# Performance work log

Hardware: AMD Instinct MI355X
Metric: run time of the kernel (lower is better)

The kernel has to match this reference:

```python
import jax, jax.numpy as jnp
import numpy as np

B, S, NB, D, H = 4, 512, 32, 512, 8

def setup_inputs() -> dict:
    key = jax.random.key(0)
    ks = jax.random.split(key, 8)
    sc = 1.0 / np.sqrt(D)
    return {
        "query": jax.random.normal(ks[0], (B, S, NB, D), dtype=jnp.float32),
        "key": jax.random.normal(ks[1], (B, S, NB, D), dtype=jnp.float32),
        "value": jax.random.normal(ks[2], (B, S, NB, D), dtype=jnp.float32),
        "padding_mask": jnp.zeros((B, S, NB), dtype=jnp.float32),
        "wq": jax.random.normal(ks[3], (D, D), dtype=jnp.float32) * sc,
        "bq": jnp.zeros((D,), dtype=jnp.float32),
        "wk": jax.random.normal(ks[4], (D, D), dtype=jnp.float32) * sc,
        "bk": jnp.zeros((D,), dtype=jnp.float32),
        "wv": jax.random.normal(ks[5], (D, D), dtype=jnp.float32) * sc,
        "bv": jnp.zeros((D,), dtype=jnp.float32),
        "nhead": H,
    }

def reference(query, key, value, padding_mask, wq, bq, wk, bk, wv, bv, nhead):
    b, s, nb, d = query.shape
    dh = d // nhead
    # Linear projections (torch Linear: x @ W.T + b)
    Q = query @ wq.T + bq
    K = key @ wk.T + bk
    V = value @ wv.T + bv
    # [B, S, Nb, H, dh] -> [B, H, S, Nb, dh]
    def split_heads(x):
        return x.reshape(b, s, nb, nhead, dh).transpose(0, 3, 1, 2, 4)
    Qh, Kh, Vh = split_heads(Q), split_heads(K), split_heads(V)
    # attention over the block axis per (batch, head, seq position)
    logits = jnp.einsum('bhsnd,bhsmd->bhsnm', Qh, Kh) / jnp.sqrt(jnp.float32(dh))
    # additive mask [B, S, Nb] -> [B, 1, S, 1, Nb]
    logits = logits + padding_mask[:, None, :, None, :]
    attn_weight = jax.nn.softmax(logits, axis=-1)  # [B,H,S,Nb,Nb]
    attn_output = jnp.einsum('bhsnm,bhsmd->bhsnd', attn_weight, Vh)
    # [B,H,S,Nb,dh] -> [B,S,Nb,H,dh] -> [B,S,Nb,D]
    attn_output = attn_output.transpose(0, 2, 3, 1, 4).reshape(b, s, nb, d)
    return (attn_output, attn_weight)
```

## Files before the change

### kernel.cpp

```cpp
#include <hip/hip_runtime.h>
#include <hip/hip_bf16.h>


#define NBD (32 * 512)
#define XH_STRIDE 260
#define XH_BYTES (32 * XH_STRIDE * 2)

typedef __bf16 bf16x8 __attribute__((ext_vector_type(8)));
typedef float f32x16 __attribute__((ext_vector_type(16)));

__device__ __forceinline__ unsigned f2b(float f) {
  union { float f; unsigned u; } v;
  v.f = f;
  return (v.u + 0x7fffu + ((v.u >> 16) & 1u)) >> 16;
}

__device__ __forceinline__ f32x16 mfma32(uint4 a, uint4 b, f32x16 c) {
  union { uint4 u; bf16x8 v; } ua, ub;
  ua.u = a;
  ub.u = b;
  return __builtin_amdgcn_mfma_f32_32x32x16_bf16(ua.v, ub.v, c, 0, 0, 0);
}

__device__ __forceinline__ uint4 ld_lds_64x2(const unsigned short* p, unsigned byteoff) {
  const char* c = (const char*)p;
  uint2 lo = *(const uint2*)(c + byteoff);
  uint2 hi = *(const uint2*)(c + byteoff + 8);
  uint4 r;
  r.x = lo.x; r.y = lo.y; r.z = hi.x; r.w = hi.y;
  return r;
}

__device__ __forceinline__ uint4 frag_cd(const unsigned* CP, int qb, int half) {
  const unsigned s0 = __shfl_xor(CP[qb + 0], 32);
  const unsigned s1 = __shfl_xor(CP[qb + 1], 32);
  const unsigned s2 = __shfl_xor(CP[qb + 2], 32);
  const unsigned s3 = __shfl_xor(CP[qb + 3], 32);
  uint4 f;
  f.x = half ? s2 : CP[qb + 0];
  f.y = half ? s3 : CP[qb + 1];
  f.z = half ? CP[qb + 2] : s0;
  f.w = half ? CP[qb + 3] : s1;
  return f;
}

__global__ void wconv_kernel(const float* __restrict__ wq,
                             const float* __restrict__ wk,
                             const float* __restrict__ wv,
                             uint4* __restrict__ out) {
  const int g = blockIdx.x * blockDim.x + threadIdx.x;
  const int m = g >> 15;
  const int j = g & 32767;
  const int l31 = j & 31;
  const int half = (j >> 5) & 1;
  const int k = (j >> 6) & 31;
  const int tile = j >> 11;
  const float* src = (m == 0) ? wq : (m == 1) ? wk : wv;
  const float4* p = (const float4*)(src + (size_t)(tile * 32 + l31) * 512 + k * 16 + half * 8);
  float4 f0 = p[0], f1 = p[1];
  uint4 o;
  o.x = f2b(f0.x) | (f2b(f0.y) << 16);
  o.y = f2b(f0.z) | (f2b(f0.w) << 16);
  o.z = f2b(f1.x) | (f2b(f1.y) << 16);
  o.w = f2b(f1.z) | (f2b(f1.w) << 16);
  out[g] = o;
}

__global__ __launch_bounds__(512, 4)
void mhba_kernel(const float* __restrict__ q_in, const float* __restrict__ k_in,
                 const float* __restrict__ v_in, const float* __restrict__ mask,
                 const float* __restrict__ bq, const float* __restrict__ bk,
                 const float* __restrict__ bv,
                 const uint4* __restrict__ wpk,
                 float* __restrict__ out_attn,
                 float* __restrict__ out_w) {
  __shared__ unsigned short Xs[2][32 * XH_STRIDE];
  __shared__ __align__(16) char SCR[8][4352];

  const int bs = blockIdx.x;
  const int tid = threadIdx.x;
  const int lane = tid & 63;
  const int h = tid >> 6;
  const int l31 = lane & 31;
  const int half = lane >> 5;

  char* scr = &SCR[h][0];
  const float* srcs[3] = {k_in, q_in, v_in};

  unsigned QT[2][8], VP[2][8];
  const unsigned abase = (unsigned)(l31 * (XH_STRIDE * 2) + half * 16);

  float4 st[4];

#define STAGE_LOAD(M, H1)                                                  \
  {                                                                        \
    const float4* s4 = (const float4*)(srcs[M] + (size_t)bs * NBD);        \
    _Pragma("unroll") for (int i = 0; i < 4; ++i) {                        \
      const int idx4 = i * 512 + tid;                                      \
      st[i] = s4[(idx4 >> 6) * 128 + (H1)*64 + (idx4 & 63)];               \
    }                                                                      \
  }

#define STAGE_WRITE(P)                                                     \
  {                                                                        \
    _Pragma("unroll") for (int i = 0; i < 4; ++i) {                        \
      const int idx4 = i * 512 + tid;                                      \
      const int n = idx4 >> 6, k4 = idx4 & 63;                             \
      uint2 u;                                                             \
      u.x = f2b(st[i].x) | (f2b(st[i].y) << 16);                           \
      u.y = f2b(st[i].z) | (f2b(st[i].w) << 16);                           \
      *(uint2*)((char*)Xs[P] + (n * (XH_STRIDE * 2) + k4 * 8)) = u;        \
    }                                                                      \
  }

#define COMPUTE_HALF(P, WSEL, H1, TRANSPOSED)                              \
  {                                                                        \
    const uint4* w0 = wpk + (WSEL)*32768 + (2 * h) * 2048 + (H1)*1024 +    \
                      half * 32 + l31;                                     \
    const uint4* w1 = w0 + 2048;                                           \
    _Pragma("unroll 8") for (int k = 0; k < 16; ++k) {                     \
      uint4 a = ld_lds_64x2(Xs[P], abase + (unsigned)k * 32);              \
      uint4 b0 = w0[k * 64];                                               \
      uint4 b1 = w1[k * 64];                                               \
      if (TRANSPOSED) {                                                    \
        acc0 = mfma32(b0, a, acc0);                                        \
        acc1 = mfma32(b1, a, acc1);                                        \
      } else {                                                             \
        acc0 = mfma32(a, b0, acc0);                                        \
        acc1 = mfma32(a, b1, acc1);                                        \
      }                                                                    \
    }                                                                      \
  }

  f32x16 acc0, acc1;
#pragma unroll
  for (int r = 0; r < 16; ++r) { acc0[r] = 0.0f; acc1[r] = 0.0f; }

  STAGE_LOAD(0, 0);
  STAGE_WRITE(0);
  __syncthreads();

  STAGE_LOAD(0, 1);
  COMPUTE_HALF(0, 1, 0, 0);
  STAGE_WRITE(1);
  __syncthreads();

  STAGE_LOAD(1, 0);
  COMPUTE_HALF(1, 1, 1, 0);
  {
    const float bc0 = bk[h * 64 + l31];
    const float bc1 = bk[h * 64 + 32 + l31];
#pragma unroll
    for (int r = 0; r < 16; ++r) {
      const int n = (r & 3) + 8 * (r >> 2) + 4 * half;
      const unsigned base = (unsigned)(n * 128);
      const unsigned sw = (unsigned)(n & 7) << 4;
      *(unsigned short*)(scr + ((base + l31 * 2) ^ sw)) =
          (unsigned short)f2b(acc0[r] + bc0);
      *(unsigned short*)(scr + ((base + 64 + l31 * 2) ^ sw)) =
          (unsigned short)f2b(acc1[r] + bc1);
      acc0[r] = 0.0f;
      acc1[r] = 0.0f;
    }
  }
  STAGE_WRITE(0);
  __syncthreads();

  STAGE_LOAD(1, 1);
  COMPUTE_HALF(0, 0, 0, 1);
  STAGE_WRITE(1);
  __syncthreads();

  STAGE_LOAD(2, 0);
  COMPUTE_HALF(1, 0, 1, 1);
  {
#pragma unroll
    for (int q = 0; q < 8; ++q) {
      const int n0 = ((2 * q) & 3) + 8 * (q >> 1) + 4 * half;
      float2 bv0 = *(const float2*)(bq + h * 64 + n0);
      float2 bv1 = *(const float2*)(bq + h * 64 + 32 + n0);
      QT[0][q] = f2b(acc0[2 * q] + bv0.x) | (f2b(acc0[2 * q + 1] + bv0.y) << 16);
      QT[1][q] = f2b(acc1[2 * q] + bv1.x) | (f2b(acc1[2 * q + 1] + bv1.y) << 16);
      acc0[2 * q] = 0.0f; acc0[2 * q + 1] = 0.0f;
      acc1[2 * q] = 0.0f; acc1[2 * q + 1] = 0.0f;
    }
  }
  STAGE_WRITE(0);
  __syncthreads();

  STAGE_LOAD(2, 1);
  COMPUTE_HALF(0, 2, 0, 0);
  STAGE_WRITE(1);
  __syncthreads();

  COMPUTE_HALF(1, 2, 1, 0);
  {
    const float bc0 = bv[h * 64 + l31];
    const float bc1 = bv[h * 64 + 32 + l31];
#pragma unroll
    for (int q = 0; q < 8; ++q) {
      VP[0][q] = f2b(acc0[2 * q] + bc0) | (f2b(acc0[2 * q + 1] + bc0) << 16);
      VP[1][q] = f2b(acc1[2 * q] + bc1) | (f2b(acc1[2 * q + 1] + bc1) << 16);
    }
  }

  uint4 KA[4];
#pragma unroll
  for (int kk = 0; kk < 4; ++kk) {
    const unsigned off =
        (unsigned)(l31 * 128 + kk * 32 + half * 16) ^ ((unsigned)(l31 & 7) << 4);
    KA[kk] = *(const uint4*)(scr + off);
  }

  f32x16 lg;
#pragma unroll
  for (int r = 0; r < 16; ++r) lg[r] = 0.0f;
#pragma unroll
  for (int kk = 0; kk < 4; ++kk) {
    uint4 qf = frag_cd(QT[kk >> 1], (kk & 1) * 4, half);
    lg = mfma32(KA[kk], qf, lg);
  }

  const float* mrow = mask + (size_t)bs * 32;
  float w[16];
#pragma unroll
  for (int q = 0; q < 8; ++q) {
    const int mm0 = ((2 * q) & 3) + 8 * (q >> 1) + 4 * half;
    float2 mk = *(const float2*)(mrow + mm0);
    w[2 * q] = lg[2 * q] * 0.125f + mk.x;
    w[2 * q + 1] = lg[2 * q + 1] * 0.125f + mk.y;
  }
  float mx = w[0];
#pragma unroll
  for (int r = 1; r < 16; ++r) mx = fmaxf(mx, w[r]);
  mx = fmaxf(mx, __shfl_xor(mx, 32));
  float ss = 0.0f;
#pragma unroll
  for (int r = 0; r < 16; ++r) {
    w[r] = __expf(w[r] - mx);
    ss += w[r];
  }
  ss += __shfl_xor(ss, 32);
  const float inv = __frcp_rn(ss);
#pragma unroll
  for (int r = 0; r < 16; ++r) w[r] *= inv;

  unsigned PP[8];
#pragma unroll
  for (int q = 0; q < 8; ++q)
    PP[q] = f2b(w[2 * q]) | (f2b(w[2 * q + 1]) << 16);

  asm volatile("" ::: "memory");
  float* scrF = (float*)scr;
#pragma unroll
  for (int r = 0; r < 16; ++r) {
    const int mm = (r & 3) + 8 * (r >> 2) + 4 * half;
    scrF[l31 * 33 + mm] = w[r];
  }
  const int b = bs >> 9;
  const int s = bs & 511;
  float* wout = out_w + ((size_t)((b * 8 + h) * 512 + s)) * 1024;
#pragma unroll
  for (int j = 0; j < 16; ++j) {
    const int n = 2 * j + half;
    wout[n * 32 + l31] = scrF[n * 33 + l31];
  }

  f32x16 o0, o1;
#pragma unroll
  for (int r = 0; r < 16; ++r) { o0[r] = 0.0f; o1[r] = 0.0f; }
#pragma unroll
  for (int kk = 0; kk < 2; ++kk) {
    uint4 pa = frag_cd(PP, 4 * kk, half);
    uint4 vb0 = frag_cd(VP[0], 4 * kk, half);
    uint4 vb1 = frag_cd(VP[1], 4 * kk, half);
    o0 = mfma32(pa, vb0, o0);
    o1 = mfma32(pa, vb1, o1);
  }

  float* obase = out_attn + (size_t)bs * NBD + h * 64 + l31;
#pragma unroll
  for (int r = 0; r < 16; ++r) {
    const int n = (r & 3) + 8 * (r >> 2) + 4 * half;
    obase[n * 512] = o0[r];
    obase[n * 512 + 32] = o1[r];
  }
#undef STAGE_LOAD
#undef STAGE_WRITE
#undef COMPUTE_HALF
}

extern "C" void kernel_launch(void* const* d_in, const int* in_sizes, int n_in,
                              void* d_out, int out_size, void* d_ws, size_t ws_size,
                              hipStream_t stream) {
  const float* q    = (const float*)d_in[0];
  const float* k    = (const float*)d_in[1];
  const float* v    = (const float*)d_in[2];
  const float* mask = (const float*)d_in[3];
  const float* wq   = (const float*)d_in[4];
  const float* bq   = (const float*)d_in[5];
  const float* wk   = (const float*)d_in[6];
  const float* bk   = (const float*)d_in[7];
  const float* wv   = (const float*)d_in[8];
  const float* bv   = (const float*)d_in[9];

  uint4* wpk = (uint4*)d_ws;
  float* out_attn = (float*)d_out;
  float* out_w = out_attn + (size_t)4 * 512 * 32 * 512;

  wconv_kernel<<<384, 256, 0, stream>>>(wq, wk, wv, wpk);
  mhba_kernel<<<2048, 512, 0, stream>>>(q, k, v, mask, bq, bk, bv, wpk,
                                        out_attn, out_w);
}
```

Baseline: 245.3 us.

## Process two sequence positions per block to reuse weight fragments

Each block now handles two (b,s) positions instead of one, so every weight fragment loaded from global memory feeds four MFMAs instead of two. The goal is to halve weight-fetch traffic per unit of work in the projection GEMMs. In exchange, registers and LDS per block double (four accumulators, doubled staging buffers), launch bounds drop to two blocks per CU, and the grid is halved. This lowers occupancy and latency hiding.

```diff
diff --git a/kernel.cpp b/kernel.cpp
--- a/kernel.cpp
+++ b/kernel.cpp
@@ -66,7 +66,7 @@
   out[g] = o;
 }
 
-__global__ __launch_bounds__(512, 4)
+__global__ __launch_bounds__(512, 2)
 void mhba_kernel(const float* __restrict__ q_in, const float* __restrict__ k_in,
                  const float* __restrict__ v_in, const float* __restrict__ mask,
                  const float* __restrict__ bq, const float* __restrict__ bk,
@@ -74,42 +74,46 @@
                  const uint4* __restrict__ wpk,
                  float* __restrict__ out_attn,
                  float* __restrict__ out_w) {
-  __shared__ unsigned short Xs[2][32 * XH_STRIDE];
-  __shared__ __align__(16) char SCR[8][4352];
-
-  const int bs = blockIdx.x;
+  __shared__ unsigned short Xs[2][2 * 32 * XH_STRIDE];
+  __shared__ __align__(16) char SCR[8][2][4352];
+
+  const int bs0 = blockIdx.x * 2;
   const int tid = threadIdx.x;
   const int lane = tid & 63;
   const int h = tid >> 6;
   const int l31 = lane & 31;
   const int half = lane >> 5;
 
-  char* scr = &SCR[h][0];
   const float* srcs[3] = {k_in, q_in, v_in};
 
-  unsigned QT[2][8], VP[2][8];
+  unsigned QT[2][2][8], VP[2][2][8];
   const unsigned abase = (unsigned)(l31 * (XH_STRIDE * 2) + half * 16);
 
-  float4 st[4];
+  float4 st[8];
 
 #define STAGE_LOAD(M, H1)                                                  \
   {                                                                        \
-    const float4* s4 = (const float4*)(srcs[M] + (size_t)bs * NBD);        \
-    _Pragma("unroll") for (int i = 0; i < 4; ++i) {                        \
-      const int idx4 = i * 512 + tid;                                      \
-      st[i] = s4[(idx4 >> 6) * 128 + (H1)*64 + (idx4 & 63)];               \
+    _Pragma("unroll") for (int j = 0; j < 2; ++j) {                        \
+      const float4* s4 = (const float4*)(srcs[M] + (size_t)(bs0 + j) * NBD);\
+      _Pragma("unroll") for (int i = 0; i < 4; ++i) {                      \
+        const int idx4 = i * 512 + tid;                                    \
+        st[j * 4 + i] = s4[(idx4 >> 6) * 128 + (H1)*64 + (idx4 & 63)];     \
+      }                                                                    \
     }                                                                      \
   }
 
 #define STAGE_WRITE(P)                                                     \
   {                                                                        \
-    _Pragma("unroll") for (int i = 0; i < 4; ++i) {                        \
-      const int idx4 = i * 512 + tid;                                      \
-      const int n = idx4 >> 6, k4 = idx4 & 63;                             \
-      uint2 u;                                                             \
-      u.x = f2b(st[i].x) | (f2b(st[i].y) << 16);                           \
-      u.y = f2b(st[i].z) | (f2b(st[i].w) << 16);                           \
-      *(uint2*)((char*)Xs[P] + (n * (XH_STRIDE * 2) + k4 * 8)) = u;        \
+    _Pragma("unroll") for (int j = 0; j < 2; ++j) {                        \
+      _Pragma("unroll") for (int i = 0; i < 4; ++i) {                      \
+        const int idx4 = i * 512 + tid;                                    \
+        const int n = idx4 >> 6, k4 = idx4 & 63;                           \
+        float4 f = st[j * 4 + i];                                          \
+        uint2 u;                                                           \
+        u.x = f2b(f.x) | (f2b(f.y) << 16);                                 \
+        u.y = f2b(f.z) | (f2b(f.w) << 16);                                 \
+        *(uint2*)((char*)Xs[P] + (j * XH_BYTES + n * (XH_STRIDE * 2) + k4 * 8)) = u; \
+      }                                                                    \
     }                                                                      \
   }
 
@@ -118,23 +122,34 @@
     const uint4* w0 = wpk + (WSEL)*32768 + (2 * h) * 2048 + (H1)*1024 +    \
                       half * 32 + l31;                                     \
     const uint4* w1 = w0 + 2048;                                           \
-    _Pragma("unroll 8") for (int k = 0; k < 16; ++k) {                     \
-      uint4 a = ld_lds_64x2(Xs[P], abase + (unsigned)k * 32);              \
+    _Pragma("unroll 4") for (int k = 0; k < 16; ++k) {                     \
       uint4 b0 = w0[k * 64];                                               \
       uint4 b1 = w1[k * 64];                                               \
+      uint4 a0 = ld_lds_64x2(Xs[P], abase + (unsigned)k * 32);             \
+      uint4 a1 = ld_lds_64x2(Xs[P], XH_BYTES + abase + (unsigned)k * 32);  \
       if (TRANSPOSED) {                                                    \
-        acc0 = mfma32(b0, a, acc0);                                        \
-        acc1 = mfma32(b1, a, acc1);                                        \
+        acc00 = mfma32(b0, a0, acc00);                                     \
+        acc01 = mfma32(b1, a0, acc01);                                     \
+        acc10 = mfma32(b0, a1, acc10);                                     \
+        acc11 = mfma32(b1, a1, acc11);                                     \
       } else {                                                             \
-        acc0 = mfma32(a, b0, acc0);                                        \
-        acc1 = mfma32(a, b1, acc1);                                        \
+        acc00 = mfma32(a0, b0, acc00);                                     \
+        acc01 = mfma32(a0, b1, acc01);                                     \
+        acc10 = mfma32(a1, b0, acc10);                                     \
+        acc11 = mfma32(a1, b1, acc11);                                     \
       }                                                                    \
     }                                                                      \
   }
 
-  f32x16 acc0, acc1;
-#pragma unroll
-  for (int r = 0; r < 16; ++r) { acc0[r] = 0.0f; acc1[r] = 0.0f; }
+#define RESET_ACCS                                                         \
+  {                                                                        \
+    _Pragma("unroll") for (int r = 0; r < 16; ++r) {                       \
+      acc00[r] = 0.0f; acc01[r] = 0.0f; acc10[r] = 0.0f; acc11[r] = 0.0f;  \
+    }                                                                      \
+  }
+
+  f32x16 acc00, acc01, acc10, acc11;
+  RESET_ACCS;
 
   STAGE_LOAD(0, 0);
   STAGE_WRITE(0);
@@ -151,17 +166,22 @@
     const float bc0 = bk[h * 64 + l31];
     const float bc1 = bk[h * 64 + 32 + l31];
 #pragma unroll
-    for (int r = 0; r < 16; ++r) {
-      const int n = (r & 3) + 8 * (r >> 2) + 4 * half;
-      const unsigned base = (unsigned)(n * 128);
-      const unsigned sw = (unsigned)(n & 7) << 4;
-      *(unsigned short*)(scr + ((base + l31 * 2) ^ sw)) =
-          (unsigned short)f2b(acc0[r] + bc0);
-      *(unsigned short*)(scr + ((base + 64 + l31 * 2) ^ sw)) =
-          (unsigned short)f2b(acc1[r] + bc1);
-      acc0[r] = 0.0f;
-      acc1[r] = 0.0f;
-    }
+    for (int j = 0; j < 2; ++j) {
+      char* scr = &SCR[h][j][0];
+#pragma unroll
+      for (int r = 0; r < 16; ++r) {
+        const int n = (r & 3) + 8 * (r >> 2) + 4 * half;
+        const unsigned base = (unsigned)(n * 128);
+        const unsigned sw = (unsigned)(n & 7) << 4;
+        const float a0 = (j == 0) ? acc00[r] : acc10[r];
+        const float a1 = (j == 0) ? acc01[r] : acc11[r];
+        *(unsigned short*)(scr + ((base + l31 * 2) ^ sw)) =
+            (unsigned short)f2b(a0 + bc0);
+        *(unsigned short*)(scr + ((base + 64 + l31 * 2) ^ sw)) =
+            (unsigned short)f2b(a1 + bc1);
+      }
+    }
+    RESET_ACCS;
   }
   STAGE_WRITE(0);
   __syncthreads();
@@ -177,13 +197,14 @@
 #pragma unroll
     for (int q = 0; q < 8; ++q) {
       const int n0 = ((2 * q) & 3) + 8 * (q >> 1) + 4 * half;
-      float2 bv0 = *(const float2*)(bq + h * 64 + n0);
-      float2 bv1 = *(const float2*)(bq + h * 64 + 32 + n0);
-      QT[0][q] = f2b(acc0[2 * q] + bv0.x) | (f2b(acc0[2 * q + 1] + bv0.y) << 16);
-      QT[1][q] = f2b(acc1[2 * q] + bv1.x) | (f2b(acc1[2 * q + 1] + bv1.y) << 16);
-      acc0[2 * q] = 0.0f; acc0[2 * q + 1] = 0.0f;
-      acc1[2 * q] = 0.0f; acc1[2 * q + 1] = 0.0f;
-    }
+      float2 b0 = *(const float2*)(bq + h * 64 + n0);
+      float2 b1 = *(const float2*)(bq + h * 64 + 32 + n0);
+      QT[0][0][q] = f2b(acc00[2 * q] + b0.x) | (f2b(acc00[2 * q + 1] + b0.y) << 16);
+      QT[0][1][q] = f2b(acc01[2 * q] + b1.x) | (f2b(acc01[2 * q + 1] + b1.y) << 16);
+      QT[1][0][q] = f2b(acc10[2 * q] + b0.x) | (f2b(acc10[2 * q + 1] + b0.y) << 16);
+      QT[1][1][q] = f2b(acc11[2 * q] + b1.x) | (f2b(acc11[2 * q + 1] + b1.y) << 16);
+    }
+    RESET_ACCS;
   }
   STAGE_WRITE(0);
   __syncthreads();
@@ -199,95 +220,104 @@
     const float bc1 = bv[h * 64 + 32 + l31];
 #pragma unroll
     for (int q = 0; q < 8; ++q) {
-      VP[0][q] = f2b(acc0[2 * q] + bc0) | (f2b(acc0[2 * q + 1] + bc0) << 16);
-      VP[1][q] = f2b(acc1[2 * q] + bc1) | (f2b(acc1[2 * q + 1] + bc1) << 16);
-    }
-  }
-
-  uint4 KA[4];
-#pragma unroll
-  for (int kk = 0; kk < 4; ++kk) {
-    const unsigned off =
-        (unsigned)(l31 * 128 + kk * 32 + half * 16) ^ ((unsigned)(l31 & 7) << 4);
-    KA[kk] = *(const uint4*)(scr + off);
-  }
-
-  f32x16 lg;
-#pragma unroll
-  for (int r = 0; r < 16; ++r) lg[r] = 0.0f;
-#pragma unroll
-  for (int kk = 0; kk < 4; ++kk) {
-    uint4 qf = frag_cd(QT[kk >> 1], (kk & 1) * 4, half);
-    lg = mfma32(KA[kk], qf, lg);
-  }
-
-  const float* mrow = mask + (size_t)bs * 32;
-  float w[16];
-#pragma unroll
-  for (int q = 0; q < 8; ++q) {
-    const int mm0 = ((2 * q) & 3) + 8 * (q >> 1) + 4 * half;
-    float2 mk = *(const float2*)(mrow + mm0);
-    w[2 * q] = lg[2 * q] * 0.125f + mk.x;
-    w[2 * q + 1] = lg[2 * q + 1] * 0.125f + mk.y;
-  }
-  float mx = w[0];
-#pragma unroll
-  for (int r = 1; r < 16; ++r) mx = fmaxf(mx, w[r]);
-  mx = fmaxf(mx, __shfl_xor(mx, 32));
-  float ss = 0.0f;
-#pragma unroll
-  for (int r = 0; r < 16; ++r) {
-    w[r] = __expf(w[r] - mx);
-    ss += w[r];
-  }
-  ss += __shfl_xor(ss, 32);
-  const float inv = __frcp_rn(ss);
-#pragma unroll
-  for (int r = 0; r < 16; ++r) w[r] *= inv;
-
-  unsigned PP[8];
-#pragma unroll
-  for (int q = 0; q < 8; ++q)
-    PP[q] = f2b(w[2 * q]) | (f2b(w[2 * q + 1]) << 16);
-
-  asm volatile("" ::: "memory");
-  float* scrF = (float*)scr;
-#pragma unroll
-  for (int r = 0; r < 16; ++r) {
-    const int mm = (r & 3) + 8 * (r >> 2) + 4 * half;
-    scrF[l31 * 33 + mm] = w[r];
-  }
-  const int b = bs >> 9;
-  const int s = bs & 511;
-  float* wout = out_w + ((size_t)((b * 8 + h) * 512 + s)) * 1024;
-#pragma unroll
-  for (int j = 0; j < 16; ++j) {
-    const int n = 2 * j + half;
-    wout[n * 32 + l31] = scrF[n * 33 + l31];
-  }
-
-  f32x16 o0, o1;
-#pragma unroll
-  for (int r = 0; r < 16; ++r) { o0[r] = 0.0f; o1[r] = 0.0f; }
-#pragma unroll
-  for (int kk = 0; kk < 2; ++kk) {
-    uint4 pa = frag_cd(PP, 4 * kk, half);
-    uint4 vb0 = frag_cd(VP[0], 4 * kk, half);
-    uint4 vb1 = frag_cd(VP[1], 4 * kk, half);
-    o0 = mfma32(pa, vb0, o0);
-    o1 = mfma32(pa, vb1, o1);
-  }
-
-  float* obase = out_attn + (size_t)bs * NBD + h * 64 + l31;
-#pragma unroll
-  for (int r = 0; r < 16; ++r) {
-    const int n = (r & 3) + 8 * (r >> 2) + 4 * half;
-    obase[n * 512] = o0[r];
-    obase[n * 512 + 32] = o1[r];
+      VP[0][0][q] = f2b(acc00[2 * q] + bc0) | (f2b(acc00[2 * q + 1] + bc0) << 16);
+      VP[0][1][q] = f2b(acc01[2 * q] + bc1) | (f2b(acc01[2 * q + 1] + bc1) << 16);
+      VP[1][0][q] = f2b(acc10[2 * q] + bc0) | (f2b(acc10[2 * q + 1] + bc0) << 16);
+      VP[1][1][q] = f2b(acc11[2 * q] + bc1) | (f2b(acc11[2 * q + 1] + bc1) << 16);
+    }
+  }
+
+#pragma unroll
+  for (int j = 0; j < 2; ++j) {
+    const int bsj = bs0 + j;
+    char* scr = &SCR[h][j][0];
+
+    uint4 KA[4];
+#pragma unroll
+    for (int kk = 0; kk < 4; ++kk) {
+      const unsigned off =
+          (unsigned)(l31 * 128 + kk * 32 + half * 16) ^ ((unsigned)(l31 & 7) << 4);
+      KA[kk] = *(const uint4*)(scr + off);
+    }
+
+    f32x16 lg;
+#pragma unroll
+    for (int r = 0; r < 16; ++r) lg[r] = 0.0f;
+#pragma unroll
+    for (int kk = 0; kk < 4; ++kk) {
+      uint4 qf = frag_cd(QT[j][kk >> 1], (kk & 1) * 4, half);
+      lg = mfma32(KA[kk], qf, lg);
+    }
+
+    const float* mrow = mask + (size_t)bsj * 32;
+    float w[16];
+#pragma unroll
+    for (int q = 0; q < 8; ++q) {
+      const int mm0 = ((2 * q) & 3) + 8 * (q >> 1) + 4 * half;
+      float2 mk = *(const float2*)(mrow + mm0);
+      w[2 * q] = lg[2 * q] * 0.125f + mk.x;
+      w[2 * q + 1] = lg[2 * q + 1] * 0.125f + mk.y;
+    }
+    float mx = w[0];
+#pragma unroll
+    for (int r = 1; r < 16; ++r) mx = fmaxf(mx, w[r]);
+    mx = fmaxf(mx, __shfl_xor(mx, 32));
+    float ss = 0.0f;
+#pragma unroll
+    for (int r = 0; r < 16; ++r) {
+      w[r] = __expf(w[r] - mx);
+      ss += w[r];
+    }
+    ss += __shfl_xor(ss, 32);
+    const float inv = __frcp_rn(ss);
+#pragma unroll
+    for (int r = 0; r < 16; ++r) w[r] *= inv;
+
+    unsigned PP[8];
+#pragma unroll
+    for (int q = 0; q < 8; ++q)
+      PP[q] = f2b(w[2 * q]) | (f2b(w[2 * q + 1]) << 16);
+
+    asm volatile("" ::: "memory");
+    float* scrF = (float*)scr;
+#pragma unroll
+    for (int r = 0; r < 16; ++r) {
+      const int mm = (r & 3) + 8 * (r >> 2) + 4 * half;
+      scrF[l31 * 33 + mm] = w[r];
+    }
+    const int b = bsj >> 9;
+    const int s = bsj & 511;
+    float* wout = out_w + ((size_t)((b * 8 + h) * 512 + s)) * 1024;
+#pragma unroll
+    for (int jj = 0; jj < 16; ++jj) {
+      const int n = 2 * jj + half;
+      wout[n * 32 + l31] = scrF[n * 33 + l31];
+    }
+
+    f32x16 o0, o1;
+#pragma unroll
+    for (int r = 0; r < 16; ++r) { o0[r] = 0.0f; o1[r] = 0.0f; }
+#pragma unroll
+    for (int kk = 0; kk < 2; ++kk) {
+      uint4 pa = frag_cd(PP, 4 * kk, half);
+      uint4 vb0 = frag_cd(VP[j][0], 4 * kk, half);
+      uint4 vb1 = frag_cd(VP[j][1], 4 * kk, half);
+      o0 = mfma32(pa, vb0, o0);
+      o1 = mfma32(pa, vb1, o1);
+    }
+
+    float* obase = out_attn + (size_t)bsj * NBD + h * 64 + l31;
+#pragma unroll
+    for (int r = 0; r < 16; ++r) {
+      const int n = (r & 3) + 8 * (r >> 2) + 4 * half;
+      obase[n * 512] = o0[r];
+      obase[n * 512 + 32] = o1[r];
+    }
   }
 #undef STAGE_LOAD
 #undef STAGE_WRITE
 #undef COMPUTE_HALF
+#undef RESET_ACCS
 }
 
 extern "C" void kernel_launch(void* const* d_in, const int* in_sizes, int n_in,
@@ -309,6 +339,6 @@
   float* out_w = out_attn + (size_t)4 * 512 * 32 * 512;
 
   wconv_kernel<<<384, 256, 0, stream>>>(wq, wk, wv, wpk);
-  mhba_kernel<<<2048, 512, 0, stream>>>(q, k, v, mask, bq, bk, bv, wpk,
+  mhba_kernel<<<1024, 512, 0, stream>>>(q, k, v, mask, bq, bk, bv, wpk,
                                         out_attn, out_w);
 }
```

Measured after the change: 231.8 us (median of 2 runs). -5.5%, faster.

## Split block into producer waves for staging and consumer waves for MFMA compute

Applied to the files above, without the earlier changes.

The block grows from 512 to 768 threads: four extra producer waves load fp32 inputs from global memory, convert them to bf16 and write them into the double-buffered LDS tile, while the eight head waves only run the MFMA projections and the attention. The aim is to take global-load latency and conversion work off the compute waves so the two overlap across the barriers. The cost is that launch bounds change to 768 threads with 3 blocks per CU, which tightens register budgets and may lower occupancy. Each producer thread now holds eight float4 loads in flight, and the compute loop unroll drops from 8 to 4.

```diff
diff --git a/kernel.cpp b/kernel.cpp
--- a/kernel.cpp
+++ b/kernel.cpp
@@ -66,7 +66,7 @@
   out[g] = o;
 }
 
-__global__ __launch_bounds__(512, 4)
+__global__ __launch_bounds__(768, 3)
 void mhba_kernel(const float* __restrict__ q_in, const float* __restrict__ k_in,
                  const float* __restrict__ v_in, const float* __restrict__ mask,
                  const float* __restrict__ bq, const float* __restrict__ bk,
@@ -80,35 +80,30 @@
   const int bs = blockIdx.x;
   const int tid = threadIdx.x;
   const int lane = tid & 63;
-  const int h = tid >> 6;
+  const int wave = tid >> 6;
   const int l31 = lane & 31;
   const int half = lane >> 5;
-
-  char* scr = &SCR[h][0];
-  const float* srcs[3] = {k_in, q_in, v_in};
+  const bool prod = (wave >= 8);
+  const int h = wave;
+  const int pid = tid - 512;
 
   unsigned QT[2][8], VP[2][8];
   const unsigned abase = (unsigned)(l31 * (XH_STRIDE * 2) + half * 16);
 
-  float4 st[4];
-
-#define STAGE_LOAD(M, H1)                                                  \
+#define PSTAGE(SRC, H1, P)                                                 \
   {                                                                        \
-    const float4* s4 = (const float4*)(srcs[M] + (size_t)bs * NBD);        \
-    _Pragma("unroll") for (int i = 0; i < 4; ++i) {                        \
-      const int idx4 = i * 512 + tid;                                      \
-      st[i] = s4[(idx4 >> 6) * 128 + (H1)*64 + (idx4 & 63)];               \
+    const float4* s4 = (const float4*)((SRC) + (size_t)bs * NBD);          \
+    float4 st[8];                                                          \
+    _Pragma("unroll") for (int ii = 0; ii < 8; ++ii) {                     \
+      const int idx4 = ii * 256 + pid;                                     \
+      st[ii] = s4[(idx4 >> 6) * 128 + (H1)*64 + (idx4 & 63)];              \
     }                                                                      \
-  }
-
-#define STAGE_WRITE(P)                                                     \
-  {                                                                        \
-    _Pragma("unroll") for (int i = 0; i < 4; ++i) {                        \
-      const int idx4 = i * 512 + tid;                                      \
+    _Pragma("unroll") for (int ii = 0; ii < 8; ++ii) {                     \
+      const int idx4 = ii * 256 + pid;                                     \
       const int n = idx4 >> 6, k4 = idx4 & 63;                             \
       uint2 u;                                                             \
-      u.x = f2b(st[i].x) | (f2b(st[i].y) << 16);                           \
-      u.y = f2b(st[i].z) | (f2b(st[i].w) << 16);                           \
+      u.x = f2b(st[ii].x) | (f2b(st[ii].y) << 16);                         \
+      u.y = f2b(st[ii].z) | (f2b(st[ii].w) << 16);                         \
       *(uint2*)((char*)Xs[P] + (n * (XH_STRIDE * 2) + k4 * 8)) = u;        \
     }                                                                      \
   }
@@ -118,7 +113,7 @@
     const uint4* w0 = wpk + (WSEL)*32768 + (2 * h) * 2048 + (H1)*1024 +    \
                       half * 32 + l31;                                     \
     const uint4* w1 = w0 + 2048;                                           \
-    _Pragma("unroll 8") for (int k = 0; k < 16; ++k) {                     \
+    _Pragma("unroll 4") for (int k = 0; k < 16; ++k) {                     \
       uint4 a = ld_lds_64x2(Xs[P], abase + (unsigned)k * 32);              \
       uint4 b0 = w0[k * 64];                                               \
       uint4 b1 = w1[k * 64];                                               \
@@ -136,18 +131,17 @@
 #pragma unroll
   for (int r = 0; r < 16; ++r) { acc0[r] = 0.0f; acc1[r] = 0.0f; }
 
-  STAGE_LOAD(0, 0);
-  STAGE_WRITE(0);
-  __syncthreads();
-
-  STAGE_LOAD(0, 1);
-  COMPUTE_HALF(0, 1, 0, 0);
-  STAGE_WRITE(1);
-  __syncthreads();
-
-  STAGE_LOAD(1, 0);
-  COMPUTE_HALF(1, 1, 1, 0);
-  {
+  if (prod) PSTAGE(k_in, 0, 0);
+  __syncthreads();
+
+  if (prod) { PSTAGE(k_in, 1, 1); } else { COMPUTE_HALF(0, 1, 0, 0); }
+  __syncthreads();
+
+  if (prod) {
+    PSTAGE(q_in, 0, 0);
+  } else {
+    COMPUTE_HALF(1, 1, 1, 0);
+    char* scr = &SCR[h][0];
     const float bc0 = bk[h * 64 + l31];
     const float bc1 = bk[h * 64 + 32 + l31];
 #pragma unroll
@@ -163,17 +157,15 @@
       acc1[r] = 0.0f;
     }
   }
-  STAGE_WRITE(0);
-  __syncthreads();
-
-  STAGE_LOAD(1, 1);
-  COMPUTE_HALF(0, 0, 0, 1);
-  STAGE_WRITE(1);
-  __syncthreads();
-
-  STAGE_LOAD(2, 0);
-  COMPUTE_HALF(1, 0, 1, 1);
-  {
+  __syncthreads();
+
+  if (prod) { PSTAGE(q_in, 1, 1); } else { COMPUTE_HALF(0, 0, 0, 1); }
+  __syncthreads();
+
+  if (prod) {
+    PSTAGE(v_in, 0, 0);
+  } else {
+    COMPUTE_HALF(1, 0, 1, 1);
 #pragma unroll
     for (int q = 0; q < 8; ++q) {
       const int n0 = ((2 * q) & 3) + 8 * (q >> 1) + 4 * half;
@@ -185,16 +177,13 @@
       acc1[2 * q] = 0.0f; acc1[2 * q + 1] = 0.0f;
     }
   }
-  STAGE_WRITE(0);
-  __syncthreads();
-
-  STAGE_LOAD(2, 1);
-  COMPUTE_HALF(0, 2, 0, 0);
-  STAGE_WRITE(1);
-  __syncthreads();
-
-  COMPUTE_HALF(1, 2, 1, 0);
-  {
+  __syncthreads();
+
+  if (prod) { PSTAGE(v_in, 1, 1); } else { COMPUTE_HALF(0, 2, 0, 0); }
+  __syncthreads();
+
+  if (!prod) {
+    COMPUTE_HALF(1, 2, 1, 0);
     const float bc0 = bv[h * 64 + l31];
     const float bc1 = bv[h * 64 + 32 + l31];
 #pragma unroll
@@ -202,91 +191,91 @@
       VP[0][q] = f2b(acc0[2 * q] + bc0) | (f2b(acc0[2 * q + 1] + bc0) << 16);
       VP[1][q] = f2b(acc1[2 * q] + bc1) | (f2b(acc1[2 * q + 1] + bc1) << 16);
     }
-  }
-
-  uint4 KA[4];
-#pragma unroll
-  for (int kk = 0; kk < 4; ++kk) {
-    const unsigned off =
-        (unsigned)(l31 * 128 + kk * 32 + half * 16) ^ ((unsigned)(l31 & 7) << 4);
-    KA[kk] = *(const uint4*)(scr + off);
-  }
-
-  f32x16 lg;
-#pragma unroll
-  for (int r = 0; r < 16; ++r) lg[r] = 0.0f;
-#pragma unroll
-  for (int kk = 0; kk < 4; ++kk) {
-    uint4 qf = frag_cd(QT[kk >> 1], (kk & 1) * 4, half);
-    lg = mfma32(KA[kk], qf, lg);
-  }
-
-  const float* mrow = mask + (size_t)bs * 32;
-  float w[16];
-#pragma unroll
-  for (int q = 0; q < 8; ++q) {
-    const int mm0 = ((2 * q) & 3) + 8 * (q >> 1) + 4 * half;
-    float2 mk = *(const float2*)(mrow + mm0);
-    w[2 * q] = lg[2 * q] * 0.125f + mk.x;
-    w[2 * q + 1] = lg[2 * q + 1] * 0.125f + mk.y;
-  }
-  float mx = w[0];
-#pragma unroll
-  for (int r = 1; r < 16; ++r) mx = fmaxf(mx, w[r]);
-  mx = fmaxf(mx, __shfl_xor(mx, 32));
-  float ss = 0.0f;
-#pragma unroll
-  for (int r = 0; r < 16; ++r) {
-    w[r] = __expf(w[r] - mx);
-    ss += w[r];
-  }
-  ss += __shfl_xor(ss, 32);
-  const float inv = __frcp_rn(ss);
-#pragma unroll
-  for (int r = 0; r < 16; ++r) w[r] *= inv;
-
-  unsigned PP[8];
-#pragma unroll
-  for (int q = 0; q < 8; ++q)
-    PP[q] = f2b(w[2 * q]) | (f2b(w[2 * q + 1]) << 16);
-
-  asm volatile("" ::: "memory");
-  float* scrF = (float*)scr;
-#pragma unroll
-  for (int r = 0; r < 16; ++r) {
-    const int mm = (r & 3) + 8 * (r >> 2) + 4 * half;
-    scrF[l31 * 33 + mm] = w[r];
-  }
-  const int b = bs >> 9;
-  const int s = bs & 511;
-  float* wout = out_w + ((size_t)((b * 8 + h) * 512 + s)) * 1024;
-#pragma unroll
-  for (int j = 0; j < 16; ++j) {
-    const int n = 2 * j + half;
-    wout[n * 32 + l31] = scrF[n * 33 + l31];
-  }
-
-  f32x16 o0, o1;
-#pragma unroll
-  for (int r = 0; r < 16; ++r) { o0[r] = 0.0f; o1[r] = 0.0f; }
-#pragma unroll
-  for (int kk = 0; kk < 2; ++kk) {
-    uint4 pa = frag_cd(PP, 4 * kk, half);
-    uint4 vb0 = frag_cd(VP[0], 4 * kk, half);
-    uint4 vb1 = frag_cd(VP[1], 4 * kk, half);
-    o0 = mfma32(pa, vb0, o0);
-    o1 = mfma32(pa, vb1, o1);
-  }
-
-  float* obase = out_attn + (size_t)bs * NBD + h * 64 + l31;
-#pragma unroll
-  for (int r = 0; r < 16; ++r) {
-    const int n = (r & 3) + 8 * (r >> 2) + 4 * half;
-    obase[n * 512] = o0[r];
-    obase[n * 512 + 32] = o1[r];
-  }
-#undef STAGE_LOAD
-#undef STAGE_WRITE
+
+    char* scr = &SCR[h][0];
+    uint4 KA[4];
+#pragma unroll
+    for (int kk = 0; kk < 4; ++kk) {
+      const unsigned off =
+          (unsigned)(l31 * 128 + kk * 32 + half * 16) ^ ((unsigned)(l31 & 7) << 4);
+      KA[kk] = *(const uint4*)(scr + off);
+    }
+
+    f32x16 lg;
+#pragma unroll
+    for (int r = 0; r < 16; ++r) lg[r] = 0.0f;
+#pragma unroll
+    for (int kk = 0; kk < 4; ++kk) {
+      uint4 qf = frag_cd(QT[kk >> 1], (kk & 1) * 4, half);
+      lg = mfma32(KA[kk], qf, lg);
+    }
+
+    const float* mrow = mask + (size_t)bs * 32;
+    float w[16];
+#pragma unroll
+    for (int q = 0; q < 8; ++q) {
+      const int mm0 = ((2 * q) & 3) + 8 * (q >> 1) + 4 * half;
+      float2 mk = *(const float2*)(mrow + mm0);
+      w[2 * q] = lg[2 * q] * 0.125f + mk.x;
+      w[2 * q + 1] = lg[2 * q + 1] * 0.125f + mk.y;
+    }
+    float mx = w[0];
+#pragma unroll
+    for (int r = 1; r < 16; ++r) mx = fmaxf(mx, w[r]);
+    mx = fmaxf(mx, __shfl_xor(mx, 32));
+    float ss = 0.0f;
+#pragma unroll
+    for (int r = 0; r < 16; ++r) {
+      w[r] = __expf(w[r] - mx);
+      ss += w[r];
+    }
+    ss += __shfl_xor(ss, 32);
+    const float inv = __frcp_rn(ss);
+#pragma unroll
+    for (int r = 0; r < 16; ++r) w[r] *= inv;
+
+    unsigned PP[8];
+#pragma unroll
+    for (int q = 0; q < 8; ++q)
+      PP[q] = f2b(w[2 * q]) | (f2b(w[2 * q + 1]) << 16);
+
+    asm volatile("" ::: "memory");
+    float* scrF = (float*)scr;
+#pragma unroll
+    for (int r = 0; r < 16; ++r) {
+      const int mm = (r & 3) + 8 * (r >> 2) + 4 * half;
+      scrF[l31 * 33 + mm] = w[r];
+    }
+    const int b = bs >> 9;
+    const int s = bs & 511;
+    float* wout = out_w + ((size_t)((b * 8 + h) * 512 + s)) * 1024;
+#pragma unroll
+    for (int j = 0; j < 16; ++j) {
+      const int n = 2 * j + half;
+      wout[n * 32 + l31] = scrF[n * 33 + l31];
+    }
+
+    f32x16 o0, o1;
+#pragma unroll
+    for (int r = 0; r < 16; ++r) { o0[r] = 0.0f; o1[r] = 0.0f; }
+#pragma unroll
+    for (int kk = 0; kk < 2; ++kk) {
+      uint4 pa = frag_cd(PP, 4 * kk, half);
+      uint4 vb0 = frag_cd(VP[0], 4 * kk, half);
+      uint4 vb1 = frag_cd(VP[1], 4 * kk, half);
+      o0 = mfma32(pa, vb0, o0);
+      o1 = mfma32(pa, vb1, o1);
+    }
+
+    float* obase = out_attn + (size_t)bs * NBD + h * 64 + l31;
+#pragma unroll
+    for (int r = 0; r < 16; ++r) {
+      const int n = (r & 3) + 8 * (r >> 2) + 4 * half;
+      obase[n * 512] = o0[r];
+      obase[n * 512 + 32] = o1[r];
+    }
+  }
+#undef PSTAGE
 #undef COMPUTE_HALF
 }
 
@@ -309,6 +298,6 @@
   float* out_w = out_attn + (size_t)4 * 512 * 32 * 512;
 
   wconv_kernel<<<384, 256, 0, stream>>>(wq, wk, wv, wpk);
-  mhba_kernel<<<2048, 512, 0, stream>>>(q, k, v, mask, bq, bk, bv, wpk,
+  mhba_kernel<<<2048, 768, 0, stream>>>(q, k, v, mask, bq, bk, bv, wpk,
                                         out_attn, out_w);
 }
```

New measurement: 284.9 us. 1.16x slower.
